# Performance work log

Hardware: AMD Instinct MI355X
Metric: run time of the kernel (lower is better)

## Reference

```python
import jax, jax.numpy as jnp
import numpy as np

N_HEADS = 8
D_HEAD = 64
IGNORE = -1.0e6  # matches the torch buffer


def setup_inputs() -> dict:
    key = jax.random.key(0)
    ks = jax.random.split(key, 9)
    B, S, D = 2, 128, 512
    H, Dh = N_HEADS, D_HEAD
    sc = lambda n: 1.0 / np.sqrt(n)
    x = jax.random.normal(ks[0], (B, S, D), jnp.float32)
    # kkq: Linear(d_model, 3*H*Dh)
    W_kkq = jax.random.normal(ks[1], (D, 3 * H * Dh), jnp.float32) * sc(D)
    b_kkq = jax.random.normal(ks[2], (3 * H * Dh,), jnp.float32) * 0.02
    # V12: Linear(2*d_model, H*Dh); split its weight into the half applied to
    # x[p] (Wv_a) and the half applied to x[s] (Wv_b) -- mathematically identical
    # to concatenating [x[p], x[s]] and applying one Linear, but avoids the
    # (B,S,S,2D) intermediate.
    Wv_a = jax.random.normal(ks[3], (D, H * Dh), jnp.float32) * sc(2 * D)
    Wv_b = jax.random.normal(ks[4], (D, H * Dh), jnp.float32) * sc(2 * D)
    b_v = jax.random.normal(ks[5], (H * Dh,), jnp.float32) * 0.02
    # Out: Linear(H*Dh, d_model)
    W_out = jax.random.normal(ks[6], (H * Dh, D), jnp.float32) * sc(H * Dh)
    b_out = jax.random.normal(ks[7], (D,), jnp.float32) * 0.02
    return {"x": x, "W_kkq": W_kkq, "b_kkq": b_kkq, "Wv_a": Wv_a,
            "Wv_b": Wv_b, "b_v": b_v, "W_out": W_out, "b_out": b_out}


def reference(x, W_kkq, b_kkq, Wv_a, Wv_b, b_v, W_out, b_out):
    B, S, D = x.shape
    H, Dh = N_HEADS, D_HEAD
    # projections
    kkq = x @ W_kkq + b_kkq                       # (B,S,3*H*Dh)
    k1, k2, q = jnp.split(kkq, 3, axis=-1)
    rs = lambda a: a.reshape(B, S, H, Dh)
    k1, k2, q = rs(k1), rs(k2), rs(q)
    # cubic tri-way scores: torch einsum 'bsnh,btnh,bqnh->bnstq' (we emit bnqst)
    scores = jnp.einsum('bsnh,btnh,bqnh->bnqst', k1, k2, q)  # (B,H,S,S,S)
    # faithful reproduction of the torch precomputed mask: only (t > q) masks
    # (the s>q term collapses to False due to the broadcast-shape bug upstream)
    idx = jnp.arange(S)
    mask_qt = idx[None, :] > idx[:, None]          # (q, t): True where t > q
    scores = jnp.where(mask_qt[None, None, :, None, :], IGNORE, scores)
    scores = scores / Dh                           # scale AFTER masking, as in torch
    # softmax jointly over the (s, t) pair axis
    A = jax.nn.softmax(scores.reshape(B, H, S, S * S), axis=-1).reshape(B, H, S, S, S)
    # values: v[p,s] = Linear([x[p], x[s]]) = x[p]@Wv_a + x[s]@Wv_b + b_v
    va = (x @ Wv_a).reshape(B, S, H, Dh)
    vb = (x @ Wv_b).reshape(B, S, H, Dh)
    # z[q] = sum_{s,t} A[q,s,t] * (va[s] + vb[t] + b_v); softmax sums to 1 so the
    # bias contributes exactly b_v
    z = (jnp.einsum('bnqst,bsnh->bqnh', A, va)
         + jnp.einsum('bnqst,btnh->bqnh', A, vb)
         + b_v.reshape(H, Dh))                     # (B,S,H,Dh)
    out = z.reshape(B, S, H * Dh) @ W_out + b_out  # (B,S,D)
    return out
```

## Files before the change

kernel.cpp:

```cpp
#include <hip/hip_runtime.h>
#include <hip/hip_bf16.h>

#define B_  2
#define S_  128
#define D_  512
#define H_  8
#define DH_ 64
#define IGNORE_VAL (-1.0e6f)
#define QB  4

#define XSF 520
#define K2S 72

#define QSCALE 0.022542110f
#define MASKED_L2 (-22542.11f)

typedef __attribute__((ext_vector_type(8))) short bf16x8;
typedef __attribute__((ext_vector_type(4))) float f32x4;
typedef __attribute__((ext_vector_type(2))) __bf16 bf16x2;

__device__ __forceinline__ unsigned short f2bf(float f) {
    __bf16 h = (__bf16)f;
    return __builtin_bit_cast(unsigned short, h);
}
__device__ __forceinline__ unsigned f2bf2(float lo, float hi) {
    bf16x2 h = { (__bf16)lo, (__bf16)hi };
    return __builtin_bit_cast(unsigned, h);
}

__global__ __launch_bounds__(256) void proj_kernel(
    const float* __restrict__ x,
    const float* __restrict__ W_kkq, const float* __restrict__ b_kkq,
    const float* __restrict__ Wv_a,  const float* __restrict__ Wv_b,
    float* __restrict__ k1_ws, unsigned short* __restrict__ k2bf, float* __restrict__ q_ws,
    float* __restrict__ va_ws, float* __restrict__ vb_ws)
{
    __shared__ __align__(16) unsigned short xs[32 * XSF];

    const int cb = blockIdx.x;
    const int rb = blockIdx.y;
    const int tid = threadIdx.x;
    const int lane = tid & 63, wvx = tid >> 6;
    const int n16 = lane & 15, quad = lane >> 4;

    const int part = cb >> 3;
    const float* Wbase; int wstride; int wcoloff;
    if (part <= 2) { Wbase = W_kkq; wstride = 1536; wcoloff = cb * 64; }
    else if (part == 3) { Wbase = Wv_a; wstride = 512; wcoloff = (cb - 24) * 64; }
    else { Wbase = Wv_b; wstride = 512; wcoloff = (cb - 32) * 64; }

    {
        const int c = (tid & 63) * 8;
#pragma unroll
        for (int i = 0; i < 8; ++i) {
            const int m = (tid >> 6) + i * 4;
            const float* src = x + (size_t)(rb * 32 + m) * D_ + c;
            const float4 a = *reinterpret_cast<const float4*>(src);
            const float4 b4 = *reinterpret_cast<const float4*>(src + 4);
            uint4 pk;
            pk.x = f2bf2(a.x,  a.y);
            pk.y = f2bf2(a.z,  a.w);
            pk.z = f2bf2(b4.x, b4.y);
            pk.w = f2bf2(b4.z, b4.w);
            *reinterpret_cast<uint4*>(&xs[m * XSF + c]) = pk;
        }
    }
    __syncthreads();

    f32x4 acc[2];
    acc[0] = (f32x4){0.f, 0.f, 0.f, 0.f};
    acc[1] = (f32x4){0.f, 0.f, 0.f, 0.f};
    const int ncol = wcoloff + wvx * 16 + n16;

#pragma unroll
    for (int ks = 0; ks < 8; ++ks) {
#pragma unroll
        for (int kk = 0; kk < 2; ++kk) {
            const int k = ks * 64 + kk * 32 + quad * 8;
            const float* wp = Wbase + (size_t)k * wstride + ncol;
            float w[8];
#pragma unroll
            for (int j = 0; j < 8; ++j) w[j] = wp[(size_t)j * wstride];
            bf16x8 bf;
            unsigned* bu = reinterpret_cast<unsigned*>(&bf);
            bu[0] = f2bf2(w[0], w[1]);
            bu[1] = f2bf2(w[2], w[3]);
            bu[2] = f2bf2(w[4], w[5]);
            bu[3] = f2bf2(w[6], w[7]);
            const bf16x8 af0 = *reinterpret_cast<const bf16x8*>(&xs[n16 * XSF + k]);
            const bf16x8 af1 = *reinterpret_cast<const bf16x8*>(&xs[(16 + n16) * XSF + k]);
            acc[0] = __builtin_amdgcn_mfma_f32_16x16x32_bf16(af0, bf, acc[0], 0, 0, 0);
            acc[1] = __builtin_amdgcn_mfma_f32_16x16x32_bf16(af1, bf, acc[1], 0, 0, 0);
        }
    }

    const int n_head = cb & 7;
    const int h = wvx * 16 + n16;
    const float bias = (part <= 2) ? b_kkq[cb * 64 + h] : 0.f;
    float* Obase = (part == 0) ? k1_ws : (part == 2) ? q_ws
                 : (part == 3) ? va_ws : vb_ws;
#pragma unroll
    for (int mt = 0; mt < 2; ++mt) {
#pragma unroll
        for (int r = 0; r < 4; ++r) {
            const int row = rb * 32 + mt * 16 + quad * 4 + r;
            const int b = row >> 7, s = row & 127;
            const size_t o = (((size_t)(b * H_ + n_head) * S_ + s) << 6) + h;
            const float val = acc[mt][r] + bias;
            if (part == 1) k2bf[o] = f2bf(val);
            else           Obase[o] = val;
        }
    }
}

__global__ __launch_bounds__(256) void tri_kernel(
    const float* __restrict__ k1_ws, const unsigned short* __restrict__ k2bf,
    const float* __restrict__ q_ws,
    const float* __restrict__ va_ws, const float* __restrict__ vb_ws,
    const float* __restrict__ b_v,
    unsigned short* __restrict__ z_bf)
{
    const int qg = blockIdx.x;
    const int n = blockIdx.y;
    const int b = blockIdx.z;
    const int head = b * H_ + n;
    const float* k1h = k1_ws + (size_t)head * S_ * DH_;
    const unsigned short* k2hb = k2bf + (size_t)head * S_ * DH_;
    const float* qh = q_ws + (size_t)head * S_ * DH_;
    const float* va_h = va_ws + (size_t)head * S_ * DH_;
    const float* vb_h = vb_ws + (size_t)head * S_ * DH_;

    __shared__ __align__(16) unsigned short k2s[S_ * K2S];
    __shared__ __align__(16) float qv[QB][DH_];
    __shared__ float Asm[QB][S_];
    __shared__ float Atm[QB][S_];
    __shared__ float Atp[QB][4][S_];
    __shared__ float reds[QB][4];
    __shared__ float zred[4][QB][DH_];

    const int tid = threadIdx.x;
    const int lane = tid & 63, wv = tid >> 6;
    const int row16 = lane & 15, quad = lane >> 4;

    if (tid < QB * DH_)
        qv[tid >> 6][tid & 63] =
            qh[(size_t)(qg + 32 * (tid >> 6)) * DH_ + (tid & 63)] * QSCALE;
#pragma unroll
    for (int it = 0; it < 4; ++it) {
        const int i8 = (tid + it * 256) * 8;
        const int r = i8 >> 6, c = i8 & 63;
        uint4 v = *reinterpret_cast<const uint4*>(k2hb + i8);
        *reinterpret_cast<uint4*>(&k2s[r * K2S + c]) = v;
    }

    float k1f[2][2][8];
#pragma unroll
    for (int mt = 0; mt < 2; ++mt) {
        const int srow = (wv * 2 + mt) * 16 + row16;
#pragma unroll
        for (int kk = 0; kk < 2; ++kk) {
            const int k = kk * 32 + quad * 8;
            const float4 u0 = *reinterpret_cast<const float4*>(k1h + (size_t)srow * DH_ + k);
            const float4 u1 = *reinterpret_cast<const float4*>(k1h + (size_t)srow * DH_ + k + 4);
            k1f[mt][kk][0] = u0.x; k1f[mt][kk][1] = u0.y; k1f[mt][kk][2] = u0.z; k1f[mt][kk][3] = u0.w;
            k1f[mt][kk][4] = u1.x; k1f[mt][kk][5] = u1.y; k1f[mt][kk][6] = u1.z; k1f[mt][kk][7] = u1.w;
        }
    }
    __syncthreads();

    for (int qq = 0; qq < QB; ++qq) {
        const int qidx = qg + 32 * qq;
        const int ntlim = qidx >> 4;

        bf16x8 afrag[2][2];
#pragma unroll
        for (int mt = 0; mt < 2; ++mt)
#pragma unroll
            for (int kk = 0; kk < 2; ++kk) {
                const int k = kk * 32 + quad * 8;
                bf16x8 f;
                unsigned* fu = reinterpret_cast<unsigned*>(&f);
                fu[0] = f2bf2(k1f[mt][kk][0] * qv[qq][k + 0], k1f[mt][kk][1] * qv[qq][k + 1]);
                fu[1] = f2bf2(k1f[mt][kk][2] * qv[qq][k + 2], k1f[mt][kk][3] * qv[qq][k + 3]);
                fu[2] = f2bf2(k1f[mt][kk][4] * qv[qq][k + 4], k1f[mt][kk][5] * qv[qq][k + 5]);
                fu[3] = f2bf2(k1f[mt][kk][6] * qv[qq][k + 6], k1f[mt][kk][7] * qv[qq][k + 7]);
                afrag[mt][kk] = f;
            }

        f32x4 acc[2][8];
#pragma unroll
        for (int mt = 0; mt < 2; ++mt)
#pragma unroll
            for (int nt = 0; nt < 8; ++nt) acc[mt][nt] = (f32x4){0.f, 0.f, 0.f, 0.f};
#pragma unroll
        for (int nt = 0; nt < 8; ++nt) {
            if (nt <= ntlim) {
#pragma unroll
                for (int kk = 0; kk < 2; ++kk) {
                    bf16x8 bfrag = *reinterpret_cast<const bf16x8*>(
                        &k2s[(nt * 16 + row16) * K2S + kk * 32 + quad * 8]);
                    acc[0][nt] = __builtin_amdgcn_mfma_f32_16x16x32_bf16(afrag[0][kk], bfrag, acc[0][nt], 0, 0, 0);
                    acc[1][nt] = __builtin_amdgcn_mfma_f32_16x16x32_bf16(afrag[1][kk], bfrag, acc[1][nt], 0, 0, 0);
                }
            }
        }

        float rs[2][4], cs[8];
#pragma unroll
        for (int nt = 0; nt < 8; ++nt) cs[nt] = 0.f;
#pragma unroll
        for (int mt = 0; mt < 2; ++mt)
#pragma unroll
            for (int r = 0; r < 4; ++r) rs[mt][r] = 0.f;
#pragma unroll
        for (int nt = 0; nt < 8; ++nt) {
            if (nt <= ntlim) {
                const int t = nt * 16 + row16;
                const bool msk = (t > qidx);
#pragma unroll
                for (int mt = 0; mt < 2; ++mt)
#pragma unroll
                    for (int r = 0; r < 4; ++r) {
                        float v = msk ? MASKED_L2 : acc[mt][nt][r];
                        float p = __builtin_amdgcn_exp2f(v);
                        rs[mt][r] += p;
                        cs[nt] += p;
                    }
            }
        }

#pragma unroll
        for (int m = 1; m < 16; m <<= 1)
#pragma unroll
            for (int mt = 0; mt < 2; ++mt)
#pragma unroll
                for (int r = 0; r < 4; ++r) rs[mt][r] += __shfl_xor(rs[mt][r], m, 64);
        if (row16 == 0) {
#pragma unroll
            for (int mt = 0; mt < 2; ++mt)
#pragma unroll
                for (int r = 0; r < 4; ++r)
                    Asm[qq][(wv * 2 + mt) * 16 + quad * 4 + r] = rs[mt][r];
        }

#pragma unroll
        for (int nt = 0; nt < 8; ++nt) {
            if (nt <= ntlim) {
#pragma unroll
                for (int m = 16; m < 64; m <<= 1) cs[nt] += __shfl_xor(cs[nt], m, 64);
            }
        }
        if (quad == 0) {
#pragma unroll
            for (int nt = 0; nt < 8; ++nt) Atp[qq][wv][nt * 16 + row16] = cs[nt];
        }

        float tot = rs[0][0] + rs[0][1] + rs[0][2] + rs[0][3]
                  + rs[1][0] + rs[1][1] + rs[1][2] + rs[1][3];
#pragma unroll
        for (int m = 16; m < 64; m <<= 1) tot += __shfl_xor(tot, m, 64);
        if (lane == 0) reds[qq][wv] = tot;
    }
    __syncthreads();

    for (int i = tid; i < QB * S_; i += 256) {
        const int qq = i >> 7, t = i & 127;
        Atm[qq][t] = Atp[qq][0][t] + Atp[qq][1][t] + Atp[qq][2][t] + Atp[qq][3][t];
    }
    __syncthreads();

    {
        const int h = tid & 63, w = tid >> 6;
        float za[QB] = {0.f, 0.f, 0.f, 0.f};
        for (int i = 0; i < 32; ++i) {
            const int s = w * 32 + i;
            const float va_v = va_h[(size_t)s * DH_ + h];
            const float vb_v = vb_h[(size_t)s * DH_ + h];
#pragma unroll
            for (int qq = 0; qq < QB; ++qq)
                za[qq] += Asm[qq][s] * va_v + Atm[qq][s] * vb_v;
        }
#pragma unroll
        for (int qq = 0; qq < QB; ++qq) zred[w][qq][h] = za[qq];
    }
    __syncthreads();

    {
        const int qq = tid >> 6, h = tid & 63;
        const float Zv = reds[qq][0] + reds[qq][1] + reds[qq][2] + reds[qq][3];
        float zv = zred[0][qq][h] + zred[1][qq][h] + zred[2][qq][h] + zred[3][qq][h];
        zv = zv / Zv + b_v[n * DH_ + h];
        z_bf[((size_t)(b * S_ + qg + 32 * qq) * (H_ * DH_)) + n * DH_ + h] = f2bf(zv);
    }
}

__global__ __launch_bounds__(256) void out_kernel(
    const unsigned short* __restrict__ z_bf,
    const float* __restrict__ W_out, const float* __restrict__ b_out,
    float* __restrict__ out)
{
    __shared__ __align__(16) unsigned short zs[16 * XSF];

    const int cb = blockIdx.x;
    const int rb = blockIdx.y;
    const int tid = threadIdx.x;
    const int lane = tid & 63, wvx = tid >> 6;
    const int n16 = lane & 15, quad = lane >> 4;

    {
        const int c = (tid & 63) * 8;
#pragma unroll
        for (int i = 0; i < 4; ++i) {
            const int m = (tid >> 6) + i * 4;
            uint4 v = *reinterpret_cast<const uint4*>(
                z_bf + (size_t)(rb * 16 + m) * 512 + c);
            *reinterpret_cast<uint4*>(&zs[m * XSF + c]) = v;
        }
    }
    __syncthreads();

    f32x4 acc = (f32x4){0.f, 0.f, 0.f, 0.f};
    const int ncol = cb * 64 + wvx * 16 + n16;

#pragma unroll
    for (int ks = 0; ks < 8; ++ks) {
#pragma unroll
        for (int kk = 0; kk < 2; ++kk) {
            const int k = ks * 64 + kk * 32 + quad * 8;
            const float* wp = W_out + (size_t)k * 512 + ncol;
            float w[8];
#pragma unroll
            for (int j = 0; j < 8; ++j) w[j] = wp[(size_t)j * 512];
            bf16x8 bf;
            unsigned* bu = reinterpret_cast<unsigned*>(&bf);
            bu[0] = f2bf2(w[0], w[1]);
            bu[1] = f2bf2(w[2], w[3]);
            bu[2] = f2bf2(w[4], w[5]);
            bu[3] = f2bf2(w[6], w[7]);
            const bf16x8 af = *reinterpret_cast<const bf16x8*>(&zs[n16 * XSF + k]);
            acc = __builtin_amdgcn_mfma_f32_16x16x32_bf16(af, bf, acc, 0, 0, 0);
        }
    }

    const float bias = b_out[ncol];
#pragma unroll
    for (int r = 0; r < 4; ++r) {
        const int row = rb * 16 + quad * 4 + r;
        out[(size_t)row * 512 + ncol] = acc[r] + bias;
    }
}

extern "C" void kernel_launch(void* const* d_in, const int* in_sizes, int n_in,
                              void* d_out, int out_size, void* d_ws, size_t ws_size,
                              hipStream_t stream) {
    const float* x     = (const float*)d_in[0];
    const float* W_kkq = (const float*)d_in[1];
    const float* b_kkq = (const float*)d_in[2];
    const float* Wv_a  = (const float*)d_in[3];
    const float* Wv_b  = (const float*)d_in[4];
    const float* b_v   = (const float*)d_in[5];
    const float* W_out = (const float*)d_in[6];
    const float* b_out = (const float*)d_in[7];
    float* out = (float*)d_out;

    const size_t HE = (size_t)B_ * H_ * S_ * DH_;
    float* ws = (float*)d_ws;
    float* k1_ws = ws;
    float* q_ws  = ws + HE;
    float* va_ws = ws + 2 * HE;
    float* vb_ws = ws + 3 * HE;
    unsigned short* k2bf = (unsigned short*)(ws + 4 * HE);
    unsigned short* z_bf = (unsigned short*)(ws + 4 * HE) + HE;

    proj_kernel<<<dim3(40, 8), 256, 0, stream>>>(x, W_kkq, b_kkq, Wv_a, Wv_b,
                                                 k1_ws, k2bf, q_ws, va_ws, vb_ws);
    tri_kernel<<<dim3(32, H_, B_), 256, 0, stream>>>(k1_ws, k2bf, q_ws,
                                                     va_ws, vb_ws, b_v, z_bf);
    out_kernel<<<dim3(8, 16), 256, 0, stream>>>(z_bf, W_out, b_out, out);
}
```

Measured before the change: 97.06 us.

## Fuse output projection into tri kernel via per-head atomic accumulation

Removes the separate out_kernel launch. Each tri block now multiplies its per-head z slice (4 queries × 64 dims) by the matching 64-row slice of W_out in fp32 and atomically adds the result into the output, with head 0 adding the bias. The output buffer is zeroed inside proj_kernel so the atomics start from zero. This saves a launch and the z round-trip through memory, but adds 8-way atomic contention per output element and redundant W_out reads across blocks, and makes the fp32 summation order nondeterministic.

Result: no change. 97.09 us (+0.0%).

```diff
diff --git a/kernel.cpp b/kernel.cpp
--- a/kernel.cpp
+++ b/kernel.cpp
@@ -33,7 +33,8 @@
     const float* __restrict__ W_kkq, const float* __restrict__ b_kkq,
     const float* __restrict__ Wv_a,  const float* __restrict__ Wv_b,
     float* __restrict__ k1_ws, unsigned short* __restrict__ k2bf, float* __restrict__ q_ws,
-    float* __restrict__ va_ws, float* __restrict__ vb_ws)
+    float* __restrict__ va_ws, float* __restrict__ vb_ws,
+    float* __restrict__ out)
 {
     __shared__ __align__(16) unsigned short xs[32 * XSF];
 
@@ -42,6 +43,12 @@
     const int tid = threadIdx.x;
     const int lane = tid & 63, wvx = tid >> 6;
     const int n16 = lane & 15, quad = lane >> 4;
+
+    {
+        const int bid = rb * 40 + cb;
+        if (bid < 256)
+            reinterpret_cast<float2*>(out)[bid * 256 + tid] = make_float2(0.f, 0.f);
+    }
 
     const int part = cb >> 3;
     const float* Wbase; int wstride; int wcoloff;
@@ -118,7 +125,8 @@
     const float* __restrict__ q_ws,
     const float* __restrict__ va_ws, const float* __restrict__ vb_ws,
     const float* __restrict__ b_v,
-    unsigned short* __restrict__ z_bf)
+    const float* __restrict__ W_out, const float* __restrict__ b_out,
+    float* __restrict__ out)
 {
     const int qg = blockIdx.x;
     const int n = blockIdx.y;
@@ -137,6 +145,7 @@
     __shared__ float Atp[QB][4][S_];
     __shared__ float reds[QB][4];
     __shared__ float zred[4][QB][DH_];
+    __shared__ __align__(16) float zfin[DH_][QB];
 
     const int tid = threadIdx.x;
     const int lane = tid & 63, wv = tid >> 6;
@@ -289,64 +298,33 @@
         const int qq = tid >> 6, h = tid & 63;
         const float Zv = reds[qq][0] + reds[qq][1] + reds[qq][2] + reds[qq][3];
         float zv = zred[0][qq][h] + zred[1][qq][h] + zred[2][qq][h] + zred[3][qq][h];
-        zv = zv / Zv + b_v[n * DH_ + h];
-        z_bf[((size_t)(b * S_ + qg + 32 * qq) * (H_ * DH_)) + n * DH_ + h] = f2bf(zv);
-    }
-}
-
-__global__ __launch_bounds__(256) void out_kernel(
-    const unsigned short* __restrict__ z_bf,
-    const float* __restrict__ W_out, const float* __restrict__ b_out,
-    float* __restrict__ out)
-{
-    __shared__ __align__(16) unsigned short zs[16 * XSF];
-
-    const int cb = blockIdx.x;
-    const int rb = blockIdx.y;
-    const int tid = threadIdx.x;
-    const int lane = tid & 63, wvx = tid >> 6;
-    const int n16 = lane & 15, quad = lane >> 4;
-
-    {
-        const int c = (tid & 63) * 8;
-#pragma unroll
-        for (int i = 0; i < 4; ++i) {
-            const int m = (tid >> 6) + i * 4;
-            uint4 v = *reinterpret_cast<const uint4*>(
-                z_bf + (size_t)(rb * 16 + m) * 512 + c);
-            *reinterpret_cast<uint4*>(&zs[m * XSF + c]) = v;
-        }
-    }
-    __syncthreads();
-
-    f32x4 acc = (f32x4){0.f, 0.f, 0.f, 0.f};
-    const int ncol = cb * 64 + wvx * 16 + n16;
-
-#pragma unroll
-    for (int ks = 0; ks < 8; ++ks) {
-#pragma unroll
-        for (int kk = 0; kk < 2; ++kk) {
-            const int k = ks * 64 + kk * 32 + quad * 8;
-            const float* wp = W_out + (size_t)k * 512 + ncol;
-            float w[8];
-#pragma unroll
-            for (int j = 0; j < 8; ++j) w[j] = wp[(size_t)j * 512];
-            bf16x8 bf;
-            unsigned* bu = reinterpret_cast<unsigned*>(&bf);
-            bu[0] = f2bf2(w[0], w[1]);
-            bu[1] = f2bf2(w[2], w[3]);
-            bu[2] = f2bf2(w[4], w[5]);
-            bu[3] = f2bf2(w[6], w[7]);
-            const bf16x8 af = *reinterpret_cast<const bf16x8*>(&zs[n16 * XSF + k]);
-            acc = __builtin_amdgcn_mfma_f32_16x16x32_bf16(af, bf, acc, 0, 0, 0);
-        }
-    }
-
-    const float bias = b_out[ncol];
-#pragma unroll
-    for (int r = 0; r < 4; ++r) {
-        const int row = rb * 16 + quad * 4 + r;
-        out[(size_t)row * 512 + ncol] = acc[r] + bias;
+        zfin[h][qq] = zv / Zv + b_v[n * DH_ + h];
+    }
+    __syncthreads();
+
+    {
+        const int c0 = tid;
+        const float* Wn = W_out + (size_t)(n * DH_) * 512;
+        float a0[QB] = {0.f, 0.f, 0.f, 0.f};
+        float a1[QB] = {0.f, 0.f, 0.f, 0.f};
+#pragma unroll 8
+        for (int k = 0; k < DH_; ++k) {
+            const float w0 = Wn[(size_t)k * 512 + c0];
+            const float w1 = Wn[(size_t)k * 512 + c0 + 256];
+            const float4 zq = *reinterpret_cast<const float4*>(&zfin[k][0]);
+            a0[0] = fmaf(zq.x, w0, a0[0]);  a1[0] = fmaf(zq.x, w1, a1[0]);
+            a0[1] = fmaf(zq.y, w0, a0[1]);  a1[1] = fmaf(zq.y, w1, a1[1]);
+            a0[2] = fmaf(zq.z, w0, a0[2]);  a1[2] = fmaf(zq.z, w1, a1[2]);
+            a0[3] = fmaf(zq.w, w0, a0[3]);  a1[3] = fmaf(zq.w, w1, a1[3]);
+        }
+        const float bo0 = (n == 0) ? b_out[c0] : 0.f;
+        const float bo1 = (n == 0) ? b_out[c0 + 256] : 0.f;
+#pragma unroll
+        for (int qq = 0; qq < QB; ++qq) {
+            const size_t row = (size_t)(b * S_ + qg + 32 * qq) * 512;
+            atomicAdd(&out[row + c0],       a0[qq] + bo0);
+            atomicAdd(&out[row + c0 + 256], a1[qq] + bo1);
+        }
     }
 }
 
@@ -370,11 +348,11 @@
     float* va_ws = ws + 2 * HE;
     float* vb_ws = ws + 3 * HE;
     unsigned short* k2bf = (unsigned short*)(ws + 4 * HE);
-    unsigned short* z_bf = (unsigned short*)(ws + 4 * HE) + HE;
 
     proj_kernel<<<dim3(40, 8), 256, 0, stream>>>(x, W_kkq, b_kkq, Wv_a, Wv_b,
-                                                 k1_ws, k2bf, q_ws, va_ws, vb_ws);
+                                                 k1_ws, k2bf, q_ws, va_ws, vb_ws,
+                                                 out);
     tri_kernel<<<dim3(32, H_, B_), 256, 0, stream>>>(k1_ws, k2bf, q_ws,
-                                                     va_ws, vb_ws, b_v, z_bf);
-    out_kernel<<<dim3(8, 16), 256, 0, stream>>>(z_bf, W_out, b_out, out);
-}
+                                                     va_ws, vb_ws, b_v,
+                                                     W_out, b_out, out);
+}
```
